# Kernel optimization log

Hardware: AMD Instinct MI355X
Metric: run time of the kernel (lower is better)

The kernel has to match this reference:

```python
import jax, jax.numpy as jnp
import numpy as np

K = 3  # number of nearest neighbors for interpolation
BIG = 1e10  # masks out cross-batch pairs in the distance matrix


def setup_inputs() -> dict:
    key = jax.random.key(0)
    ks = jax.random.split(key, 8)
    N, Ns, C, Cs, B = 4096, 16384, 256, 128, 4
    Din, H = C + Cs, 256
    return {
        "x": jax.random.normal(ks[0], (N, C), dtype=jnp.float32),
        "pos": jax.random.normal(ks[1], (N, 3), dtype=jnp.float32),
        "batch": jnp.sort(jax.random.randint(ks[2], (N,), 0, B)),
        "x_skip": jax.random.normal(ks[3], (Ns, Cs), dtype=jnp.float32),
        "pos_skip": jax.random.normal(ks[4], (Ns, 3), dtype=jnp.float32),
        "batch_skip": jnp.sort(jax.random.randint(ks[5], (Ns,), 0, B)),
        "W1": jax.random.normal(ks[6], (Din, H), dtype=jnp.float32) * (1.0 / np.sqrt(Din)),
        "b1": jnp.zeros((H,), dtype=jnp.float32),
        "W2": jax.random.normal(ks[7], (H, H), dtype=jnp.float32) * (1.0 / np.sqrt(H)),
        "b2": jnp.zeros((H,), dtype=jnp.float32),
    }


def reference(x, pos, batch, x_skip, pos_skip, batch_skip, W1, b1, W2, b2):
    # knn_interpolate: squared distances from each fine point to all coarse points,
    # masked so neighbors only come from the same batch element.
    d2 = jnp.sum((pos_skip[:, None, :] - pos[None, :, :]) ** 2, axis=-1)  # [Ns, N]
    d2 = jnp.where(batch_skip[:, None] != batch[None, :], BIG, d2)
    neg_d2, idx = jax.lax.top_k(-d2, K)          # k smallest distances, [Ns, K]
    w = 1.0 / jnp.clip(-neg_d2, 1e-16)           # inverse-squared-distance weights
    num = jnp.sum(x[idx] * w[..., None], axis=1)  # [Ns, C] weighted gather-reduce
    y = num / jnp.sum(w, axis=1, keepdims=True)
    # concat skip features, then MLP (Linear-ReLU-Linear-ReLU)
    y = jnp.concatenate([y, x_skip], axis=1)      # [Ns, C + Cs]
    h = jax.nn.relu(y @ W1 + b1)
    out = jax.nn.relu(h @ W2 + b2)
    return (out, pos_skip, batch_skip)
```

## Files before the change

### kernel.cpp

```cpp
#include <hip/hip_runtime.h>
#include <stdint.h>

#define NPTS   4096
#define NSKIP  16384
#define CCH    256
#define CSK    128
#define DIN    384
#define HDIM   256
#define BIGF   1e10f

typedef unsigned short u16;
typedef __attribute__((ext_vector_type(8))) short short8;
typedef __attribute__((ext_vector_type(4))) float floatx4;

__device__ __forceinline__ u16 f2bf(float f) {
    union { float f; uint32_t u; } c; c.f = f;
    uint32_t u = c.u;
    return (u16)((u + 0x7FFFu + ((u >> 16) & 1u)) >> 16);
}

__device__ __forceinline__ double pkkey(float d, int j) {
    return __hiloint2double(__float_as_int(d), j);
}

__global__ __launch_bounds__(256) void prep_knn_kernel(
    const float* __restrict__ W1, const float* __restrict__ W2,
    u16* __restrict__ W1p, u16* __restrict__ W2p,
    const float* __restrict__ pos, const int* __restrict__ batch,
    const float* __restrict__ pos_skip, const int* __restrict__ batch_skip,
    int* __restrict__ idx3, float* __restrict__ w3)
{
    const int bid = blockIdx.x;
    const int t = threadIdx.x;

    if (bid < 80) {
        const float* W = (bid < 48) ? W1 : W2;
        u16* Wp       = (bid < 48) ? W1p : W2p;
        const int KT  = (bid < 48) ? 12 : 8;
        const int g   = ((bid < 48) ? bid : (bid - 48)) * 256 + t;

        const int lane = g & 63;
        const int kt = (g >> 6) % KT;
        const int nt = (g >> 6) / KT;
        const int kbase = kt * 32 + (lane >> 4) * 8;
        const int n = nt * 16 + (lane & 15);
        u16 v[8];
#pragma unroll
        for (int j = 0; j < 8; ++j) v[j] = f2bf(W[(size_t)(kbase + j) * HDIM + n]);
#pragma unroll
        for (int j = 0; j < 8; ++j) Wp[(size_t)g * 8 + j] = v[j];
        return;
    }

    __shared__ int sRange[5];
    if (t < 5) {
        int lo = 0, hi = NPTS;
        while (lo < hi) {
            const int m = (lo + hi) >> 1;
            if (batch[m] < t) lo = m + 1; else hi = m;
        }
        sRange[t] = lo;
    }
    __syncthreads();

    const int i = (bid - 80) * 8 + (t >> 5);
    const int sub = t & 31;
    const int b = batch_skip[i];
    const int start = sRange[b], end = sRange[b + 1];

    const float px = pos_skip[i * 3 + 0];
    const float py = pos_skip[i * 3 + 1];
    const float pz = pos_skip[i * 3 + 2];

    const double BIGKEY = pkkey(BIGF, 0x7FFFFFFF);
    double k0 = BIGKEY, k1 = BIGKEY, k2 = BIGKEY;

    for (int j = start + sub; j < end; j += 32) {
        const float qx = pos[j * 3 + 0];
        const float qy = pos[j * 3 + 1];
        const float qz = pos[j * 3 + 2];
        const float dx = __fsub_rn(px, qx);
        const float dy = __fsub_rn(py, qy);
        const float dz = __fsub_rn(pz, qz);
        const float dd = __fadd_rn(__fadd_rn(__fmul_rn(dx, dx), __fmul_rn(dy, dy)),
                                   __fmul_rn(dz, dz));
        const double kk = pkkey(dd, j);
        const double u0 = fmax(k0, kk); k0 = fmin(k0, kk);
        const double u1 = fmax(k1, u0); k1 = fmin(k1, u0);
        k2 = fmin(k2, u1);
    }

#pragma unroll
    for (int m = 1; m < 32; m <<= 1) {
        const double o0 = __shfl_xor(k0, m);
        const double o1 = __shfl_xor(k1, m);
        const double o2 = __shfl_xor(k2, m);
        double u0 = fmax(k0, o0); k0 = fmin(k0, o0);
        double u1 = fmax(k1, u0); k1 = fmin(k1, u0);
        k2 = fmin(k2, u1);
        u1 = fmax(k1, o1); k1 = fmin(k1, o1);
        k2 = fmin(k2, u1);
        k2 = fmin(k2, o2);
    }

    if (sub == 0) {
        const float d0 = __int_as_float(__double2hiint(k0));
        const float d1 = __int_as_float(__double2hiint(k1));
        const float d2 = __int_as_float(__double2hiint(k2));
        const float w0 = 1.0f / fmaxf(d0, 1e-16f);
        const float w1 = 1.0f / fmaxf(d1, 1e-16f);
        const float w2 = 1.0f / fmaxf(d2, 1e-16f);
        const float inv = 1.0f / (w0 + w1 + w2);
        idx3[i * 3 + 0] = __double2loint(k0);
        idx3[i * 3 + 1] = __double2loint(k1);
        idx3[i * 3 + 2] = __double2loint(k2);
        w3[i * 3 + 0] = w0 * inv; w3[i * 3 + 1] = w1 * inv; w3[i * 3 + 2] = w2 * inv;
    }
}

__global__ __launch_bounds__(256) void fused_mlp_kernel(
    const float* __restrict__ x, const float* __restrict__ x_skip,
    const int* __restrict__ idx3, const float* __restrict__ w3,
    const u16* __restrict__ W1p, const float* __restrict__ b1,
    const u16* __restrict__ W2p, const float* __restrict__ b2,
    const float* __restrict__ pos_skip, const int* __restrict__ batch_skip,
    float* __restrict__ out)
{
    __shared__ u16 sA[32 * 392];
    const int t = threadIdx.x;
    const int row0 = blockIdx.x * 32;

#pragma unroll
    for (int k = 0; k < 8; ++k) {
        const int g = t + 256 * k;
        const int row = g >> 6, c4 = g & 63;
        const int R = row0 + row;
        const int i0 = idx3[R * 3 + 0], i1 = idx3[R * 3 + 1], i2 = idx3[R * 3 + 2];
        const float w0 = w3[R * 3 + 0], w1 = w3[R * 3 + 1], w2 = w3[R * 3 + 2];
        const float4 v0 = *(const float4*)(x + (size_t)i0 * CCH + c4 * 4);
        const float4 v1 = *(const float4*)(x + (size_t)i1 * CCH + c4 * 4);
        const float4 v2 = *(const float4*)(x + (size_t)i2 * CCH + c4 * 4);
        const float a  = w0 * v0.x + w1 * v1.x + w2 * v2.x;
        const float bq = w0 * v0.y + w1 * v1.y + w2 * v2.y;
        const float cq = w0 * v0.z + w1 * v1.z + w2 * v2.z;
        const float dq = w0 * v0.w + w1 * v1.w + w2 * v2.w;
        uint2 pk;
        pk.x = (uint32_t)f2bf(a)  | ((uint32_t)f2bf(bq) << 16);
        pk.y = (uint32_t)f2bf(cq) | ((uint32_t)f2bf(dq) << 16);
        *(uint2*)(sA + row * 392 + c4 * 4) = pk;
    }
#pragma unroll
    for (int k = 0; k < 4; ++k) {
        const int g = t + 256 * k;
        const int row = g >> 5, c4 = g & 31;
        const float4 v = *(const float4*)(x_skip + (size_t)(row0 + row) * CSK + c4 * 4);
        uint2 pk;
        pk.x = (uint32_t)f2bf(v.x) | ((uint32_t)f2bf(v.y) << 16);
        pk.y = (uint32_t)f2bf(v.z) | ((uint32_t)f2bf(v.w) << 16);
        *(uint2*)(sA + row * 392 + CCH + c4 * 4) = pk;
    }
    __syncthreads();

    const int wave = t >> 6, lane = t & 63;
    const int quad = lane >> 4, ml = lane & 15;

    floatx4 acc[2][4] = {};
    {
        const u16* aA = sA + ml * 392 + quad * 8;
        for (int kt = 0; kt < 12; ++kt) {
            short8 a0 = *(const short8*)(aA + kt * 32);
            short8 a1 = *(const short8*)(aA + 16 * 392 + kt * 32);
#pragma unroll
            for (int nt = 0; nt < 4; ++nt) {
                const int ntile = wave * 4 + nt;
                short8 bfr = *(const short8*)(W1p + (size_t)((ntile * 12 + kt) * 64 + lane) * 8);
                acc[0][nt] = __builtin_amdgcn_mfma_f32_16x16x32_bf16(a0, bfr, acc[0][nt], 0, 0, 0);
                acc[1][nt] = __builtin_amdgcn_mfma_f32_16x16x32_bf16(a1, bfr, acc[1][nt], 0, 0, 0);
            }
        }
    }
    __syncthreads();

#pragma unroll
    for (int mt = 0; mt < 2; ++mt) {
#pragma unroll
        for (int nt = 0; nt < 4; ++nt) {
            const int n = (wave * 4 + nt) * 16 + ml;
            const float bv = b1[n];
#pragma unroll
            for (int r = 0; r < 4; ++r) {
                const int m = mt * 16 + quad * 4 + r;
                sA[m * 264 + n] = f2bf(fmaxf(acc[mt][nt][r] + bv, 0.0f));
            }
        }
    }
    __syncthreads();

    floatx4 acc2[2][4] = {};
    {
        const u16* aH = sA + ml * 264 + quad * 8;
        for (int kt = 0; kt < 8; ++kt) {
            short8 a0 = *(const short8*)(aH + kt * 32);
            short8 a1 = *(const short8*)(aH + 16 * 264 + kt * 32);
#pragma unroll
            for (int nt = 0; nt < 4; ++nt) {
                const int ntile = wave * 4 + nt;
                short8 bfr = *(const short8*)(W2p + (size_t)((ntile * 8 + kt) * 64 + lane) * 8);
                acc2[0][nt] = __builtin_amdgcn_mfma_f32_16x16x32_bf16(a0, bfr, acc2[0][nt], 0, 0, 0);
                acc2[1][nt] = __builtin_amdgcn_mfma_f32_16x16x32_bf16(a1, bfr, acc2[1][nt], 0, 0, 0);
            }
        }
    }

#pragma unroll
    for (int mt = 0; mt < 2; ++mt) {
#pragma unroll
        for (int nt = 0; nt < 4; ++nt) {
            const int n = (wave * 4 + nt) * 16 + ml;
            const float bv = b2[n];
#pragma unroll
            for (int r = 0; r < 4; ++r) {
                const int m = row0 + mt * 16 + quad * 4 + r;
                out[(size_t)m * HDIM + n] = fmaxf(acc2[mt][nt][r] + bv, 0.0f);
            }
        }
    }

    if (t < 128) {
        const int e = blockIdx.x * 128 + t;
        const size_t base = (size_t)NSKIP * HDIM;
        if (e < NSKIP * 3) out[base + e] = pos_skip[e];
        else               out[base + e] = (float)batch_skip[e - NSKIP * 3];
    }
}

extern "C" void kernel_launch(void* const* d_in, const int* in_sizes, int n_in,
                              void* d_out, int out_size, void* d_ws, size_t ws_size,
                              hipStream_t stream) {
    const float* x         = (const float*)d_in[0];
    const float* pos       = (const float*)d_in[1];
    const int*   batch     = (const int*)d_in[2];
    const float* x_skip    = (const float*)d_in[3];
    const float* pos_skip  = (const float*)d_in[4];
    const int*   batch_skip= (const int*)d_in[5];
    const float* W1        = (const float*)d_in[6];
    const float* b1        = (const float*)d_in[7];
    const float* W2        = (const float*)d_in[8];
    const float* b2        = (const float*)d_in[9];
    float* out = (float*)d_out;

    char* ws = (char*)d_ws;
    u16*    W1p   = (u16*)ws;
    u16*    W2p   = (u16*)(ws + 196608);
    int*    idx3  = (int*)(ws + 327680);
    float*  w3    = (float*)(ws + 524288);

    prep_knn_kernel<<<80 + NSKIP / 8, 256, 0, stream>>>(W1, W2, W1p, W2p,
                                                        pos, batch,
                                                        pos_skip, batch_skip,
                                                        idx3, w3);
    fused_mlp_kernel<<<NSKIP / 32, 256, 0, stream>>>(x, x_skip, idx3, w3,
                                                     W1p, b1, W2p, b2,
                                                     pos_skip, batch_skip, out);
}
```

Before: 118.0 us.

## Halve MLP row tile to 16 and batch gather loads before compute

The fused MLP kernel now handles 16 rows per block instead of 32, doubling the grid to 1024 blocks and halving LDS and accumulator use, with a launch-bounds hint of 4 blocks per CU. The gather of the three neighbor rows and the skip features is split so all global loads are issued up front before the weighted sum and bf16 packing. The aim is more parallelism and latency hiding in the gather-heavy prologue. The trade-off is that each W1/W2 B-fragment loaded from global memory now feeds one MFMA instead of two, so weight traffic per output row doubles.

```diff
diff --git a/kernel.cpp b/kernel.cpp
--- a/kernel.cpp
+++ b/kernel.cpp
@@ -118,7 +118,7 @@
     }
 }
 
-__global__ __launch_bounds__(256) void fused_mlp_kernel(
+__global__ __launch_bounds__(256, 4) void fused_mlp_kernel(
     const float* __restrict__ x, const float* __restrict__ x_skip,
     const int* __restrict__ idx3, const float* __restrict__ w3,
     const u16* __restrict__ W1p, const float* __restrict__ b1,
@@ -126,37 +126,50 @@
     const float* __restrict__ pos_skip, const int* __restrict__ batch_skip,
     float* __restrict__ out)
 {
-    __shared__ u16 sA[32 * 392];
+    __shared__ u16 sA[16 * 392];
     const int t = threadIdx.x;
-    const int row0 = blockIdx.x * 32;
-
-#pragma unroll
-    for (int k = 0; k < 8; ++k) {
+    const int row0 = blockIdx.x * 16;
+
+    float4 v0[4], v1[4], v2[4];
+    float w0r[4], w1r[4], w2r[4];
+    int rowA[4], c4A[4];
+#pragma unroll
+    for (int k = 0; k < 4; ++k) {
         const int g = t + 256 * k;
         const int row = g >> 6, c4 = g & 63;
+        rowA[k] = row; c4A[k] = c4;
         const int R = row0 + row;
         const int i0 = idx3[R * 3 + 0], i1 = idx3[R * 3 + 1], i2 = idx3[R * 3 + 2];
-        const float w0 = w3[R * 3 + 0], w1 = w3[R * 3 + 1], w2 = w3[R * 3 + 2];
-        const float4 v0 = *(const float4*)(x + (size_t)i0 * CCH + c4 * 4);
-        const float4 v1 = *(const float4*)(x + (size_t)i1 * CCH + c4 * 4);
-        const float4 v2 = *(const float4*)(x + (size_t)i2 * CCH + c4 * 4);
-        const float a  = w0 * v0.x + w1 * v1.x + w2 * v2.x;
-        const float bq = w0 * v0.y + w1 * v1.y + w2 * v2.y;
-        const float cq = w0 * v0.z + w1 * v1.z + w2 * v2.z;
-        const float dq = w0 * v0.w + w1 * v1.w + w2 * v2.w;
+        w0r[k] = w3[R * 3 + 0]; w1r[k] = w3[R * 3 + 1]; w2r[k] = w3[R * 3 + 2];
+        v0[k] = *(const float4*)(x + (size_t)i0 * CCH + c4 * 4);
+        v1[k] = *(const float4*)(x + (size_t)i1 * CCH + c4 * 4);
+        v2[k] = *(const float4*)(x + (size_t)i2 * CCH + c4 * 4);
+    }
+    float4 vs[2];
+#pragma unroll
+    for (int k = 0; k < 2; ++k) {
+        const int g = t + 256 * k;
+        const int row = g >> 5, c4 = g & 31;
+        vs[k] = *(const float4*)(x_skip + (size_t)(row0 + row) * CSK + c4 * 4);
+    }
+#pragma unroll
+    for (int k = 0; k < 4; ++k) {
+        const float a  = w0r[k] * v0[k].x + w1r[k] * v1[k].x + w2r[k] * v2[k].x;
+        const float bq = w0r[k] * v0[k].y + w1r[k] * v1[k].y + w2r[k] * v2[k].y;
+        const float cq = w0r[k] * v0[k].z + w1r[k] * v1[k].z + w2r[k] * v2[k].z;
+        const float dq = w0r[k] * v0[k].w + w1r[k] * v1[k].w + w2r[k] * v2[k].w;
         uint2 pk;
         pk.x = (uint32_t)f2bf(a)  | ((uint32_t)f2bf(bq) << 16);
         pk.y = (uint32_t)f2bf(cq) | ((uint32_t)f2bf(dq) << 16);
-        *(uint2*)(sA + row * 392 + c4 * 4) = pk;
-    }
-#pragma unroll
-    for (int k = 0; k < 4; ++k) {
+        *(uint2*)(sA + rowA[k] * 392 + c4A[k] * 4) = pk;
+    }
+#pragma unroll
+    for (int k = 0; k < 2; ++k) {
         const int g = t + 256 * k;
         const int row = g >> 5, c4 = g & 31;
-        const float4 v = *(const float4*)(x_skip + (size_t)(row0 + row) * CSK + c4 * 4);
         uint2 pk;
-        pk.x = (uint32_t)f2bf(v.x) | ((uint32_t)f2bf(v.y) << 16);
-        pk.y = (uint32_t)f2bf(v.z) | ((uint32_t)f2bf(v.w) << 16);
+        pk.x = (uint32_t)f2bf(vs[k].x) | ((uint32_t)f2bf(vs[k].y) << 16);
+        pk.y = (uint32_t)f2bf(vs[k].z) | ((uint32_t)f2bf(vs[k].w) << 16);
         *(uint2*)(sA + row * 392 + CCH + c4 * 4) = pk;
     }
     __syncthreads();
@@ -164,70 +177,60 @@
     const int wave = t >> 6, lane = t & 63;
     const int quad = lane >> 4, ml = lane & 15;
 
-    floatx4 acc[2][4] = {};
+    floatx4 acc[4] = {};
     {
         const u16* aA = sA + ml * 392 + quad * 8;
         for (int kt = 0; kt < 12; ++kt) {
             short8 a0 = *(const short8*)(aA + kt * 32);
-            short8 a1 = *(const short8*)(aA + 16 * 392 + kt * 32);
 #pragma unroll
             for (int nt = 0; nt < 4; ++nt) {
                 const int ntile = wave * 4 + nt;
                 short8 bfr = *(const short8*)(W1p + (size_t)((ntile * 12 + kt) * 64 + lane) * 8);
-                acc[0][nt] = __builtin_amdgcn_mfma_f32_16x16x32_bf16(a0, bfr, acc[0][nt], 0, 0, 0);
-                acc[1][nt] = __builtin_amdgcn_mfma_f32_16x16x32_bf16(a1, bfr, acc[1][nt], 0, 0, 0);
+                acc[nt] = __builtin_amdgcn_mfma_f32_16x16x32_bf16(a0, bfr, acc[nt], 0, 0, 0);
             }
         }
     }
     __syncthreads();
 
 #pragma unroll
-    for (int mt = 0; mt < 2; ++mt) {
-#pragma unroll
-        for (int nt = 0; nt < 4; ++nt) {
-            const int n = (wave * 4 + nt) * 16 + ml;
-            const float bv = b1[n];
-#pragma unroll
-            for (int r = 0; r < 4; ++r) {
-                const int m = mt * 16 + quad * 4 + r;
-                sA[m * 264 + n] = f2bf(fmaxf(acc[mt][nt][r] + bv, 0.0f));
-            }
-        }
-    }
-    __syncthreads();
-
-    floatx4 acc2[2][4] = {};
+    for (int nt = 0; nt < 4; ++nt) {
+        const int n = (wave * 4 + nt) * 16 + ml;
+        const float bv = b1[n];
+#pragma unroll
+        for (int r = 0; r < 4; ++r) {
+            const int m = quad * 4 + r;
+            sA[m * 264 + n] = f2bf(fmaxf(acc[nt][r] + bv, 0.0f));
+        }
+    }
+    __syncthreads();
+
+    floatx4 acc2[4] = {};
     {
         const u16* aH = sA + ml * 264 + quad * 8;
         for (int kt = 0; kt < 8; ++kt) {
             short8 a0 = *(const short8*)(aH + kt * 32);
-            short8 a1 = *(const short8*)(aH + 16 * 264 + kt * 32);
 #pragma unroll
             for (int nt = 0; nt < 4; ++nt) {
                 const int ntile = wave * 4 + nt;
                 short8 bfr = *(const short8*)(W2p + (size_t)((ntile * 8 + kt) * 64 + lane) * 8);
-                acc2[0][nt] = __builtin_amdgcn_mfma_f32_16x16x32_bf16(a0, bfr, acc2[0][nt], 0, 0, 0);
-                acc2[1][nt] = __builtin_amdgcn_mfma_f32_16x16x32_bf16(a1, bfr, acc2[1][nt], 0, 0, 0);
+                acc2[nt] = __builtin_amdgcn_mfma_f32_16x16x32_bf16(a0, bfr, acc2[nt], 0, 0, 0);
             }
         }
     }
 
 #pragma unroll
-    for (int mt = 0; mt < 2; ++mt) {
-#pragma unroll
-        for (int nt = 0; nt < 4; ++nt) {
-            const int n = (wave * 4 + nt) * 16 + ml;
-            const float bv = b2[n];
-#pragma unroll
-            for (int r = 0; r < 4; ++r) {
-                const int m = row0 + mt * 16 + quad * 4 + r;
-                out[(size_t)m * HDIM + n] = fmaxf(acc2[mt][nt][r] + bv, 0.0f);
-            }
-        }
-    }
-
-    if (t < 128) {
-        const int e = blockIdx.x * 128 + t;
+    for (int nt = 0; nt < 4; ++nt) {
+        const int n = (wave * 4 + nt) * 16 + ml;
+        const float bv = b2[n];
+#pragma unroll
+        for (int r = 0; r < 4; ++r) {
+            const int m = row0 + quad * 4 + r;
+            out[(size_t)m * HDIM + n] = fmaxf(acc2[nt][r] + bv, 0.0f);
+        }
+    }
+
+    if (t < 64) {
+        const int e = blockIdx.x * 64 + t;
         const size_t base = (size_t)NSKIP * HDIM;
         if (e < NSKIP * 3) out[base + e] = pos_skip[e];
         else               out[base + e] = (float)batch_skip[e - NSKIP * 3];
@@ -259,7 +262,7 @@
                                                         pos, batch,
                                                         pos_skip, batch_skip,
                                                         idx3, w3);
-    fused_mlp_kernel<<<NSKIP / 32, 256, 0, stream>>>(x, x_skip, idx3, w3,
+    fused_mlp_kernel<<<NSKIP / 16, 256, 0, stream>>>(x, x_skip, idx3, w3,
                                                      W1p, b1, W2p, b2,
                                                      pos_skip, batch_skip, out);
 }
```

New measurement: 118.7 us. Within noise of the previous version (+0.6%).

## Split gather-interpolate into separate kernel writing bf16 A matrix

Applied to the files above, without the earlier changes.

Moves the kNN weighted gather and x_skip bf16 conversion out of the MLP kernel into a standalone gather kernel that writes a padded bf16 activation matrix to workspace, one wave per row. The MLP kernel then does a plain coalesced copy of its 32-row tile into shared memory. The aim is more parallelism and better latency hiding for the scattered gather loads. The cost is an extra kernel launch and a round trip of the intermediate matrix through global memory.

```diff
diff --git a/kernel.cpp b/kernel.cpp
--- a/kernel.cpp
+++ b/kernel.cpp
@@ -118,9 +118,38 @@
     }
 }
 
-__global__ __launch_bounds__(256) void fused_mlp_kernel(
+__global__ __launch_bounds__(256) void gather_kernel(
     const float* __restrict__ x, const float* __restrict__ x_skip,
     const int* __restrict__ idx3, const float* __restrict__ w3,
+    u16* __restrict__ A)
+{
+    const int t = threadIdx.x;
+    const int wave = t >> 6, lane = t & 63;
+    const int row = blockIdx.x * 4 + wave;
+
+    const int i0 = idx3[row * 3 + 0], i1 = idx3[row * 3 + 1], i2 = idx3[row * 3 + 2];
+    const float w0 = w3[row * 3 + 0], w1 = w3[row * 3 + 1], w2 = w3[row * 3 + 2];
+
+    const float4 v0 = *(const float4*)(x + (size_t)i0 * CCH + lane * 4);
+    const float4 v1 = *(const float4*)(x + (size_t)i1 * CCH + lane * 4);
+    const float4 v2 = *(const float4*)(x + (size_t)i2 * CCH + lane * 4);
+    const float2 vs = *(const float2*)(x_skip + (size_t)row * CSK + lane * 2);
+
+    const float a  = w0 * v0.x + w1 * v1.x + w2 * v2.x;
+    const float bq = w0 * v0.y + w1 * v1.y + w2 * v2.y;
+    const float cq = w0 * v0.z + w1 * v1.z + w2 * v2.z;
+    const float dq = w0 * v0.w + w1 * v1.w + w2 * v2.w;
+    uint2 pk;
+    pk.x = (uint32_t)f2bf(a)  | ((uint32_t)f2bf(bq) << 16);
+    pk.y = (uint32_t)f2bf(cq) | ((uint32_t)f2bf(dq) << 16);
+    *(uint2*)(A + (size_t)row * 392 + lane * 4) = pk;
+
+    const uint32_t pks = (uint32_t)f2bf(vs.x) | ((uint32_t)f2bf(vs.y) << 16);
+    *(uint32_t*)(A + (size_t)row * 392 + CCH + lane * 2) = pks;
+}
+
+__global__ __launch_bounds__(256) void mlp_kernel(
+    const u16* __restrict__ A,
     const u16* __restrict__ W1p, const float* __restrict__ b1,
     const u16* __restrict__ W2p, const float* __restrict__ b2,
     const float* __restrict__ pos_skip, const int* __restrict__ batch_skip,
@@ -130,34 +159,11 @@
     const int t = threadIdx.x;
     const int row0 = blockIdx.x * 32;
 
-#pragma unroll
-    for (int k = 0; k < 8; ++k) {
-        const int g = t + 256 * k;
-        const int row = g >> 6, c4 = g & 63;
-        const int R = row0 + row;
-        const int i0 = idx3[R * 3 + 0], i1 = idx3[R * 3 + 1], i2 = idx3[R * 3 + 2];
-        const float w0 = w3[R * 3 + 0], w1 = w3[R * 3 + 1], w2 = w3[R * 3 + 2];
-        const float4 v0 = *(const float4*)(x + (size_t)i0 * CCH + c4 * 4);
-        const float4 v1 = *(const float4*)(x + (size_t)i1 * CCH + c4 * 4);
-        const float4 v2 = *(const float4*)(x + (size_t)i2 * CCH + c4 * 4);
-        const float a  = w0 * v0.x + w1 * v1.x + w2 * v2.x;
-        const float bq = w0 * v0.y + w1 * v1.y + w2 * v2.y;
-        const float cq = w0 * v0.z + w1 * v1.z + w2 * v2.z;
-        const float dq = w0 * v0.w + w1 * v1.w + w2 * v2.w;
-        uint2 pk;
-        pk.x = (uint32_t)f2bf(a)  | ((uint32_t)f2bf(bq) << 16);
-        pk.y = (uint32_t)f2bf(cq) | ((uint32_t)f2bf(dq) << 16);
-        *(uint2*)(sA + row * 392 + c4 * 4) = pk;
-    }
-#pragma unroll
-    for (int k = 0; k < 4; ++k) {
-        const int g = t + 256 * k;
-        const int row = g >> 5, c4 = g & 31;
-        const float4 v = *(const float4*)(x_skip + (size_t)(row0 + row) * CSK + c4 * 4);
-        uint2 pk;
-        pk.x = (uint32_t)f2bf(v.x) | ((uint32_t)f2bf(v.y) << 16);
-        pk.y = (uint32_t)f2bf(v.z) | ((uint32_t)f2bf(v.w) << 16);
-        *(uint2*)(sA + row * 392 + CCH + c4 * 4) = pk;
+    {
+        const char* src = (const char*)(A + (size_t)row0 * 392);
+        char* dst = (char*)sA;
+        for (int off = t * 16; off < 32 * 392 * 2; off += 256 * 16)
+            *(uint4*)(dst + off) = *(const uint4*)(src + off);
     }
     __syncthreads();
 
@@ -254,12 +260,13 @@
     u16*    W2p   = (u16*)(ws + 196608);
     int*    idx3  = (int*)(ws + 327680);
     float*  w3    = (float*)(ws + 524288);
+    u16*    A     = (u16*)(ws + 720896);
 
     prep_knn_kernel<<<80 + NSKIP / 8, 256, 0, stream>>>(W1, W2, W1p, W2p,
                                                         pos, batch,
                                                         pos_skip, batch_skip,
                                                         idx3, w3);
-    fused_mlp_kernel<<<NSKIP / 32, 256, 0, stream>>>(x, x_skip, idx3, w3,
-                                                     W1p, b1, W2p, b2,
-                                                     pos_skip, batch_skip, out);
-}
+    gather_kernel<<<NSKIP / 4, 256, 0, stream>>>(x, x_skip, idx3, w3, A);
+    mlp_kernel<<<NSKIP / 32, 256, 0, stream>>>(A, W1p, b1, W2p, b2,
+                                               pos_skip, batch_skip, out);
+}
```

After: 126.4 us. 7.1% more time.

## Batch gather loads, double-buffer weight fragments, and stage output through LDS

Applied to the files above, without the earlier changes.

The gather phase now issues all index, weight and feature loads for four rows before computing, so more memory requests are in flight at once. Weight B-fragments for both GEMMs are double-buffered in registers and prefetched two k-steps ahead, with the k-loops fully unrolled. The final output is written to a shared-memory tile and then stored as coalesced float4 rows instead of scattered scalar stores. This adds 32KB of LDS and more registers per thread, which may lower occupancy.

```diff
diff --git a/kernel.cpp b/kernel.cpp
--- a/kernel.cpp
+++ b/kernel.cpp
@@ -127,59 +127,102 @@
     float* __restrict__ out)
 {
     __shared__ u16 sA[32 * 392];
+    __shared__ float sOut[32 * 256];
     const int t = threadIdx.x;
     const int row0 = blockIdx.x * 32;
-
-#pragma unroll
-    for (int k = 0; k < 8; ++k) {
-        const int g = t + 256 * k;
-        const int row = g >> 6, c4 = g & 63;
-        const int R = row0 + row;
-        const int i0 = idx3[R * 3 + 0], i1 = idx3[R * 3 + 1], i2 = idx3[R * 3 + 2];
-        const float w0 = w3[R * 3 + 0], w1 = w3[R * 3 + 1], w2 = w3[R * 3 + 2];
-        const float4 v0 = *(const float4*)(x + (size_t)i0 * CCH + c4 * 4);
-        const float4 v1 = *(const float4*)(x + (size_t)i1 * CCH + c4 * 4);
-        const float4 v2 = *(const float4*)(x + (size_t)i2 * CCH + c4 * 4);
-        const float a  = w0 * v0.x + w1 * v1.x + w2 * v2.x;
-        const float bq = w0 * v0.y + w1 * v1.y + w2 * v2.y;
-        const float cq = w0 * v0.z + w1 * v1.z + w2 * v2.z;
-        const float dq = w0 * v0.w + w1 * v1.w + w2 * v2.w;
-        uint2 pk;
-        pk.x = (uint32_t)f2bf(a)  | ((uint32_t)f2bf(bq) << 16);
-        pk.y = (uint32_t)f2bf(cq) | ((uint32_t)f2bf(dq) << 16);
-        *(uint2*)(sA + row * 392 + c4 * 4) = pk;
-    }
-#pragma unroll
-    for (int k = 0; k < 4; ++k) {
-        const int g = t + 256 * k;
-        const int row = g >> 5, c4 = g & 31;
-        const float4 v = *(const float4*)(x_skip + (size_t)(row0 + row) * CSK + c4 * 4);
-        uint2 pk;
-        pk.x = (uint32_t)f2bf(v.x) | ((uint32_t)f2bf(v.y) << 16);
-        pk.y = (uint32_t)f2bf(v.z) | ((uint32_t)f2bf(v.w) << 16);
-        *(uint2*)(sA + row * 392 + CCH + c4 * 4) = pk;
-    }
-    __syncthreads();
-
     const int wave = t >> 6, lane = t & 63;
     const int quad = lane >> 4, ml = lane & 15;
+
+#pragma unroll
+    for (int half = 0; half < 2; ++half) {
+        int i0a[4], i1a[4], i2a[4];
+        float wa[4], wb[4], wc[4];
+#pragma unroll
+        for (int k = 0; k < 4; ++k) {
+            const int g = t + 256 * (half * 4 + k);
+            const int R = row0 + (g >> 6);
+            i0a[k] = idx3[R * 3 + 0]; i1a[k] = idx3[R * 3 + 1]; i2a[k] = idx3[R * 3 + 2];
+            wa[k] = w3[R * 3 + 0]; wb[k] = w3[R * 3 + 1]; wc[k] = w3[R * 3 + 2];
+        }
+        float4 v0[4], v1[4], v2[4];
+#pragma unroll
+        for (int k = 0; k < 4; ++k) {
+            const int g = t + 256 * (half * 4 + k);
+            const int c4 = g & 63;
+            v0[k] = *(const float4*)(x + (size_t)i0a[k] * CCH + c4 * 4);
+            v1[k] = *(const float4*)(x + (size_t)i1a[k] * CCH + c4 * 4);
+            v2[k] = *(const float4*)(x + (size_t)i2a[k] * CCH + c4 * 4);
+        }
+#pragma unroll
+        for (int k = 0; k < 4; ++k) {
+            const int g = t + 256 * (half * 4 + k);
+            const int row = g >> 6, c4 = g & 63;
+            const float a  = wa[k] * v0[k].x + wb[k] * v1[k].x + wc[k] * v2[k].x;
+            const float bq = wa[k] * v0[k].y + wb[k] * v1[k].y + wc[k] * v2[k].y;
+            const float cq = wa[k] * v0[k].z + wb[k] * v1[k].z + wc[k] * v2[k].z;
+            const float dq = wa[k] * v0[k].w + wb[k] * v1[k].w + wc[k] * v2[k].w;
+            uint2 pk;
+            pk.x = (uint32_t)f2bf(a)  | ((uint32_t)f2bf(bq) << 16);
+            pk.y = (uint32_t)f2bf(cq) | ((uint32_t)f2bf(dq) << 16);
+            *(uint2*)(sA + row * 392 + c4 * 4) = pk;
+        }
+    }
+    {
+        float4 vs[4];
+#pragma unroll
+        for (int k = 0; k < 4; ++k) {
+            const int g = t + 256 * k;
+            const int row = g >> 5, c4 = g & 31;
+            vs[k] = *(const float4*)(x_skip + (size_t)(row0 + row) * CSK + c4 * 4);
+        }
+#pragma unroll
+        for (int k = 0; k < 4; ++k) {
+            const int g = t + 256 * k;
+            const int row = g >> 5, c4 = g & 31;
+            uint2 pk;
+            pk.x = (uint32_t)f2bf(vs[k].x) | ((uint32_t)f2bf(vs[k].y) << 16);
+            pk.y = (uint32_t)f2bf(vs[k].z) | ((uint32_t)f2bf(vs[k].w) << 16);
+            *(uint2*)(sA + row * 392 + CCH + c4 * 4) = pk;
+        }
+    }
+    __syncthreads();
 
     floatx4 acc[2][4] = {};
     {
         const u16* aA = sA + ml * 392 + quad * 8;
+        short8 bbuf[2][4];
+#pragma unroll
+        for (int nt = 0; nt < 4; ++nt) {
+            bbuf[0][nt] = *(const short8*)(W1p + (size_t)(((wave * 4 + nt) * 12 + 0) * 64 + lane) * 8);
+            bbuf[1][nt] = *(const short8*)(W1p + (size_t)(((wave * 4 + nt) * 12 + 1) * 64 + lane) * 8);
+        }
+#pragma unroll
         for (int kt = 0; kt < 12; ++kt) {
+            short8 use[4];
+#pragma unroll
+            for (int nt = 0; nt < 4; ++nt) use[nt] = bbuf[kt & 1][nt];
+            if (kt + 2 < 12) {
+#pragma unroll
+                for (int nt = 0; nt < 4; ++nt)
+                    bbuf[kt & 1][nt] = *(const short8*)(W1p + (size_t)(((wave * 4 + nt) * 12 + kt + 2) * 64 + lane) * 8);
+            }
             short8 a0 = *(const short8*)(aA + kt * 32);
             short8 a1 = *(const short8*)(aA + 16 * 392 + kt * 32);
 #pragma unroll
             for (int nt = 0; nt < 4; ++nt) {
-                const int ntile = wave * 4 + nt;
-                short8 bfr = *(const short8*)(W1p + (size_t)((ntile * 12 + kt) * 64 + lane) * 8);
-                acc[0][nt] = __builtin_amdgcn_mfma_f32_16x16x32_bf16(a0, bfr, acc[0][nt], 0, 0, 0);
-                acc[1][nt] = __builtin_amdgcn_mfma_f32_16x16x32_bf16(a1, bfr, acc[1][nt], 0, 0, 0);
-            }
-        }
-    }
-    __syncthreads();
+                acc[0][nt] = __builtin_amdgcn_mfma_f32_16x16x32_bf16(a0, use[nt], acc[0][nt], 0, 0, 0);
+                acc[1][nt] = __builtin_amdgcn_mfma_f32_16x16x32_bf16(a1, use[nt], acc[1][nt], 0, 0, 0);
+            }
+        }
+    }
+    __syncthreads();
+
+    short8 b2buf[2][4];
+#pragma unroll
+    for (int nt = 0; nt < 4; ++nt) {
+        b2buf[0][nt] = *(const short8*)(W2p + (size_t)(((wave * 4 + nt) * 8 + 0) * 64 + lane) * 8);
+        b2buf[1][nt] = *(const short8*)(W2p + (size_t)(((wave * 4 + nt) * 8 + 1) * 64 + lane) * 8);
+    }
 
 #pragma unroll
     for (int mt = 0; mt < 2; ++mt) {
@@ -199,15 +242,22 @@
     floatx4 acc2[2][4] = {};
     {
         const u16* aH = sA + ml * 264 + quad * 8;
+#pragma unroll
         for (int kt = 0; kt < 8; ++kt) {
+            short8 use[4];
+#pragma unroll
+            for (int nt = 0; nt < 4; ++nt) use[nt] = b2buf[kt & 1][nt];
+            if (kt + 2 < 8) {
+#pragma unroll
+                for (int nt = 0; nt < 4; ++nt)
+                    b2buf[kt & 1][nt] = *(const short8*)(W2p + (size_t)(((wave * 4 + nt) * 8 + kt + 2) * 64 + lane) * 8);
+            }
             short8 a0 = *(const short8*)(aH + kt * 32);
             short8 a1 = *(const short8*)(aH + 16 * 264 + kt * 32);
 #pragma unroll
             for (int nt = 0; nt < 4; ++nt) {
-                const int ntile = wave * 4 + nt;
-                short8 bfr = *(const short8*)(W2p + (size_t)((ntile * 8 + kt) * 64 + lane) * 8);
-                acc2[0][nt] = __builtin_amdgcn_mfma_f32_16x16x32_bf16(a0, bfr, acc2[0][nt], 0, 0, 0);
-                acc2[1][nt] = __builtin_amdgcn_mfma_f32_16x16x32_bf16(a1, bfr, acc2[1][nt], 0, 0, 0);
+                acc2[0][nt] = __builtin_amdgcn_mfma_f32_16x16x32_bf16(a0, use[nt], acc2[0][nt], 0, 0, 0);
+                acc2[1][nt] = __builtin_amdgcn_mfma_f32_16x16x32_bf16(a1, use[nt], acc2[1][nt], 0, 0, 0);
             }
         }
     }
@@ -220,9 +270,18 @@
             const float bv = b2[n];
 #pragma unroll
             for (int r = 0; r < 4; ++r) {
-                const int m = row0 + mt * 16 + quad * 4 + r;
-                out[(size_t)m * HDIM + n] = fmaxf(acc2[mt][nt][r] + bv, 0.0f);
-            }
+                const int m = mt * 16 + quad * 4 + r;
+                sOut[m * 256 + n] = fmaxf(acc2[mt][nt][r] + bv, 0.0f);
+            }
+        }
+    }
+    __syncthreads();
+    {
+        float* dst = out + (size_t)row0 * HDIM;
+#pragma unroll
+        for (int k = 0; k < 8; ++k) {
+            const int e = t + 256 * k;
+            *(float4*)(dst + e * 4) = *(const float4*)(sOut + e * 4);
         }
     }
 
```

Measured after the change: 118.5 us. No clear change (+0.4%).
